# Optimization experiments

Hardware: AMD Instinct MI355X
Metric: run time of the kernel (lower is better)

Reference implementation:

```python
import jax, jax.numpy as jnp
import numpy as np

B, DIM, T = 8, 1024, 4096
CB, CD = 4096, 8          # codebook_size, codebook_dim
COMMIT = 0.25
EPS = 1e-12


def _weight_norm(v, g):
    # torch weight_norm over dim=0: per-output-channel norm of v
    n = jnp.sqrt(jnp.sum(v * v, axis=1, keepdims=True))
    return g[:, None] * v / n


def _l2_normalize(x):
    n = jnp.sqrt(jnp.sum(x * x, axis=1, keepdims=True))
    return x / jnp.maximum(n, EPS)


def setup_inputs() -> dict:
    key = jax.random.key(0)
    ks = jax.random.split(key, 5)
    z = jax.random.normal(ks[0], (B, DIM, T), jnp.float32)
    v_in = jax.random.normal(ks[1], (CD, DIM), jnp.float32) * 0.02   # conv1d k=1 weight (squeezed)
    g_in = jnp.sqrt(jnp.sum(v_in * v_in, axis=1))                     # weight_norm init: g = ||v||
    b_in = jnp.zeros((CD,), jnp.float32)
    codebook = jax.random.normal(ks[2], (CB, CD), jnp.float32)        # nn.Embedding default N(0,1)
    v_out = jax.random.normal(ks[3], (DIM, CD), jnp.float32) * 0.02
    g_out = jnp.sqrt(jnp.sum(v_out * v_out, axis=1))
    b_out = jnp.zeros((DIM,), jnp.float32)
    return {"z": z, "v_in": v_in, "g_in": g_in, "b_in": b_in,
            "codebook": codebook, "v_out": v_out, "g_out": g_out, "b_out": b_out}


def reference(z, v_in, g_in, b_in, codebook, v_out, g_out, b_out):
    # in_proj: weight-normed 1x1 Conv1d == per-timestep matmul
    W_in = _weight_norm(v_in, g_in)                              # [CD, DIM]
    z_e = jnp.einsum('od,bdt->bot', W_in, z) + b_in[None, :, None]  # [B, CD, T]

    # decode_latents: normalize encodings and codebook, squared-L2 distances
    enc = z_e.transpose(0, 2, 1).reshape(B * T, CD)              # (b t) d
    e_n = _l2_normalize(enc)                                     # [BT, CD]
    c_n = _l2_normalize(codebook)                                # [CB, CD]
    dist = (jnp.sum(e_n * e_n, axis=1, keepdims=True)
            - 2.0 * (e_n @ c_n.T)
            + jnp.sum(c_n * c_n, axis=1)[None, :])               # [BT, CB]
    indices = jnp.argmin(dist, axis=1).reshape(B, T)             # [B, T] int

    # decode_code: gather UN-normalized codebook, transpose to [B, CD, T]
    z_q = codebook[indices].transpose(0, 2, 1)                   # [B, CD, T]

    # training losses (per-batch), commitment + codebook
    sg = jax.lax.stop_gradient
    commitment_loss = jnp.mean((z_e - sg(z_q)) ** 2, axis=(1, 2)) * COMMIT
    codebook_loss = jnp.mean((z_q - sg(z_e)) ** 2, axis=(1, 2))
    commit_loss = commitment_loss + codebook_loss                # [B]

    # straight-through estimator
    z_q_ste = z_e + sg(z_q - z_e)                                # [B, CD, T]

    # out_proj
    W_out = _weight_norm(v_out, g_out)                           # [DIM, CD]
    out = jnp.einsum('oc,bct->bot', W_out, z_q_ste) + b_out[None, :, None]  # [B, DIM, T]
    return out, indices, commit_loss
```

## Files before the change

kernel.cpp:

```cpp
#include <hip/hip_runtime.h>

#define DIMN 1024
#define TN 4096
#define BN 8
#define CBN 4096
#define BTN (BN*TN)
#define OUT_ELEMS (BN*DIMN*TN)

typedef float fx4 __attribute__((ext_vector_type(4)));
typedef float fx2 __attribute__((ext_vector_type(2)));

#define WS_WINT 0
#define WS_WOUT 8192
#define WS_C2   49152
#define WS_CNP  53248
#define WS_LOSS 86016
#define WS_CNT  86024

#define LROWS_F 8192
#define LROW    68
#define LZQ_F   12544
#define LDS_TOT 13056

__device__ __forceinline__ float dot4(float4 a, float4 b) {
    float d = a.x * b.x;
    d = fmaf(a.y, b.y, d);
    d = fmaf(a.z, b.z, d);
    d = fmaf(a.w, b.w, d);
    return d;
}
__device__ __forceinline__ void add4(float4& a, float4 b) {
    a.x += b.x; a.y += b.y; a.z += b.z; a.w += b.w;
}
__device__ __forceinline__ fx2 lo2(fx4 v) { return __builtin_shufflevector(v, v, 0, 1); }
__device__ __forceinline__ fx2 hi2(fx4 v) { return __builtin_shufflevector(v, v, 2, 3); }
__device__ __forceinline__ fx2 splat2(float x) { fx2 r; r.x = x; r.y = x; return r; }
__device__ __forceinline__ fx2 fma2(fx2 a, fx2 b, fx2 c) { return __builtin_elementwise_fma(a, b, c); }
__device__ __forceinline__ fx2 max2(fx2 a, fx2 b) { return __builtin_elementwise_max(a, b); }
__device__ __forceinline__ fx2 min2(fx2 a, fx2 b) { return __builtin_elementwise_min(a, b); }
__device__ __forceinline__ fx4 cat4(fx2 a, fx2 b) { return __builtin_shufflevector(a, b, 0, 1, 2, 3); }

__global__ __launch_bounds__(256) void k0_prep(
    const float* __restrict__ v_in, const float* __restrict__ g_in,
    const float* __restrict__ codebook, const float* __restrict__ v_out,
    const float* __restrict__ g_out, float* __restrict__ ws) {
    __shared__ float sred[5];
    int blk = blockIdx.x, tid = threadIdx.x;
    if (blk < 8) {
        int o = blk;
        const float* v = v_in + o * DIMN;
        float4 x = *(const float4*)(v + tid * 4);
        float p = x.x * x.x + x.y * x.y + x.z * x.z + x.w * x.w;
        for (int off = 32; off >= 1; off >>= 1) p += __shfl_down(p, off, 64);
        if ((tid & 63) == 0) sred[tid >> 6] = p;
        __syncthreads();
        if (tid == 0) {
            float tot = sred[0] + sred[1] + sred[2] + sred[3];
            sred[4] = g_in[o] / sqrtf(tot);
        }
        __syncthreads();
        float s = sred[4];
        ws[WS_WINT + (tid * 4 + 0) * 8 + o] = x.x * s;
        ws[WS_WINT + (tid * 4 + 1) * 8 + o] = x.y * s;
        ws[WS_WINT + (tid * 4 + 2) * 8 + o] = x.z * s;
        ws[WS_WINT + (tid * 4 + 3) * 8 + o] = x.w * s;
    } else if (blk < 12) {
        int r = (blk - 8) * 256 + tid;
        const float* v = v_out + r * 8;
        float4 a = *(const float4*)v;
        float4 b = *(const float4*)(v + 4);
        float n2 = dot4(a, a) + dot4(b, b);
        float s = g_out[r] / sqrtf(n2);
        *(float4*)(ws + WS_WOUT + r * 8)     = make_float4(a.x*s, a.y*s, a.z*s, a.w*s);
        *(float4*)(ws + WS_WOUT + r * 8 + 4) = make_float4(b.x*s, b.y*s, b.z*s, b.w*s);
    } else if (blk < 28) {
        int j = (blk - 12) * 256 + tid;
        const float* c = codebook + j * 8;
        float4 a = *(const float4*)c;
        float4 b = *(const float4*)(c + 4);
        float n2 = dot4(a, a) + dot4(b, b);
        float inv = 1.0f / fmaxf(sqrtf(n2), 1e-12f);
        float na[8] = {a.x*inv, a.y*inv, a.z*inv, a.w*inv,
                       b.x*inv, b.y*inv, b.z*inv, b.w*inv};
        float* dst = ws + WS_CNP + (size_t)(j >> 1) * 16 + (j & 1);
        #pragma unroll
        for (int i = 0; i < 8; i++) dst[i * 2] = na[i];
        float h = 0.0f;
        #pragma unroll
        for (int i = 0; i < 8; i++) h = fmaf(na[i], na[i], h);
        ws[WS_C2 + j] = -0.5f * h;
    } else {
        if (tid < 9) ws[WS_LOSS + tid] = 0.0f;
    }
}

__global__ __launch_bounds__(512, 4) void k_mega(
    const float* __restrict__ z, const float* __restrict__ b_in,
    const float* __restrict__ codebook, const float* __restrict__ b_out,
    float* __restrict__ dout, float* __restrict__ ws) {
    __shared__ float sp[LDS_TOT];
    int tid = threadIdx.x, blk = blockIdx.x;
    int b = blk >> 6;
    int t0 = (blk & 63) * 64;

    #pragma unroll
    for (int i = 0; i < 4; i++) {
        int f4 = tid + i * 512;
        *(fx4*)(sp + f4 * 4) = *(const fx4*)(ws + WS_WINT + f4 * 4);
    }
    __syncthreads();

    if (tid < 256) {
        int p = tid >> 5, tpair = tid & 31;
        int tA = tpair * 2;
        const float* zp = z + ((size_t)(b * DIMN + p * 128)) * TN + t0 + tA;
        fx2 a0aL = splat2(0.f), a0aH = splat2(0.f), a0bL = splat2(0.f), a0bH = splat2(0.f);
        fx2 a1aL = splat2(0.f), a1aH = splat2(0.f), a1bL = splat2(0.f), a1bH = splat2(0.f);
        #pragma unroll 8
        for (int dd = 0; dd < 128; ++dd) {
            fx2 zv = __builtin_nontemporal_load((const fx2*)(zp + (size_t)dd * TN));
            const float* wv = sp + (p * 128 + dd) * 8;
            fx4 w0 = *(const fx4*)wv;
            fx4 w1 = *(const fx4*)(wv + 4);
            fx2 zx = splat2(zv.x), zy = splat2(zv.y);
            a0aL = fma2(lo2(w0), zx, a0aL); a0aH = fma2(hi2(w0), zx, a0aH);
            a0bL = fma2(lo2(w1), zx, a0bL); a0bH = fma2(hi2(w1), zx, a0bH);
            a1aL = fma2(lo2(w0), zy, a1aL); a1aH = fma2(hi2(w0), zy, a1aH);
            a1bL = fma2(lo2(w1), zy, a1bL); a1bH = fma2(hi2(w1), zy, a1bH);
        }
        float* q0 = sp + LROWS_F + tA * LROW + p * 8;
        *(fx4*)(q0)     = cat4(a0aL, a0aH);
        *(fx4*)(q0 + 4) = cat4(a0bL, a0bH);
        float* q1 = sp + LROWS_F + (tA + 1) * LROW + p * 8;
        *(fx4*)(q1)     = cat4(a1aL, a1aH);
        *(fx4*)(q1 + 4) = cat4(a1bL, a1bH);
    }
    __syncthreads();

    if (tid < 64) {
        int t = tid;
        float4 za = *(const float4*)(b_in);
        float4 zb = *(const float4*)(b_in + 4);
        #pragma unroll
        for (int p = 0; p < 8; p++) {
            const float* pp = sp + LROWS_F + t * LROW + p * 8;
            add4(za, *(const float4*)(pp));
            add4(zb, *(const float4*)(pp + 4));
        }
        float* row = sp + LROWS_F + t * LROW;
        *(float4*)(row)     = za;
        *(float4*)(row + 4) = zb;
        float inv = 1.0f / fmaxf(sqrtf(dot4(za, za) + dot4(zb, zb)), 1e-12f);
        *(float4*)(row + 8)  = make_float4(za.x*inv, za.y*inv, za.z*inv, za.w*inv);
        *(float4*)(row + 12) = make_float4(zb.x*inv, zb.y*inv, zb.z*inv, zb.w*inv);
    }
    __syncthreads();

    int co = tid >> 4, tg = tid & 15;
    float en[4][8];
    #pragma unroll
    for (int k = 0; k < 4; k++) {
        const float* rp = sp + LROWS_F + (tg * 4 + k) * LROW + 8;
        fx4 u = *(const fx4*)rp;
        fx4 v = *(const fx4*)(rp + 4);
        en[k][0]=u.x; en[k][1]=u.y; en[k][2]=u.z; en[k][3]=u.w;
        en[k][4]=v.x; en[k][5]=v.y; en[k][6]=v.z; en[k][7]=v.w;
    }
    fx2 bs[4]; int bje[4], bjo[4];
    #pragma unroll
    for (int k = 0; k < 4; k++) { bs[k] = splat2(-3.4e38f); bje[k] = 0; bjo[k] = 1; }
    #pragma unroll 1
    for (int ci = 0; ci < 16; ++ci) {
        int j0 = ci * 256 + co * 8;
        const float* cg = ws + WS_CNP + (size_t)j0 * 8;
        #pragma unroll
        for (int pp = 0; pp < 4; ++pp) {
            fx4 cA = *(const fx4*)(cg + pp * 16);
            fx4 cB = *(const fx4*)(cg + pp * 16 + 4);
            fx4 cC = *(const fx4*)(cg + pp * 16 + 8);
            fx4 cD = *(const fx4*)(cg + pp * 16 + 12);
            fx2 h2 = *(const fx2*)(ws + WS_C2 + j0 + pp * 2);
            int jE = j0 + pp * 2;
            #pragma unroll
            for (int k = 0; k < 4; k++) {
                fx2 s = h2;
                s = fma2(splat2(en[k][0]), lo2(cA), s);
                s = fma2(splat2(en[k][1]), hi2(cA), s);
                s = fma2(splat2(en[k][2]), lo2(cB), s);
                s = fma2(splat2(en[k][3]), hi2(cB), s);
                s = fma2(splat2(en[k][4]), lo2(cC), s);
                s = fma2(splat2(en[k][5]), hi2(cC), s);
                s = fma2(splat2(en[k][6]), lo2(cD), s);
                s = fma2(splat2(en[k][7]), hi2(cD), s);
                bool cE = s.x > bs[k].x;
                bool cO = s.y > bs[k].y;
                bs[k] = max2(bs[k], s);
                if (cE) bje[k] = jE;
                if (cO) bjo[k] = jE + 1;
            }
        }
    }
    float bsF[4]; int bjF[4];
    #pragma unroll
    for (int k = 0; k < 4; k++) {
        bsF[k] = bs[k].x; bjF[k] = bje[k];
        if (bs[k].y > bsF[k] || (bs[k].y == bsF[k] && bjo[k] < bjF[k])) {
            bsF[k] = bs[k].y; bjF[k] = bjo[k];
        }
    }
    #pragma unroll
    for (int st = 16; st <= 32; st <<= 1) {
        #pragma unroll
        for (int k = 0; k < 4; k++) {
            float os = __shfl_xor(bsF[k], st, 64);
            int   oj = __shfl_xor(bjF[k], st, 64);
            if (os > bsF[k] || (os == bsF[k] && oj < bjF[k])) { bsF[k] = os; bjF[k] = oj; }
        }
    }
    if ((tid & 63) < 16) {
        int w = tid >> 6;
        #pragma unroll
        for (int k = 0; k < 4; k++)
            *(fx2*)(sp + LROWS_F + (tg * 4 + k) * LROW + 32 + w * 2) =
                (fx2){bsF[k], __int_as_float(bjF[k])};
    }
    __syncthreads();

    if (tid < 64) {
        int t = tid;
        const float* crow = sp + LROWS_F + t * LROW + 32;
        fx2 c0 = *(const fx2*)(crow);
        float best = c0.x; int idx = __float_as_int(c0.y);
        #pragma unroll
        for (int w2 = 1; w2 < 8; w2++) {
            fx2 cw = *(const fx2*)(crow + w2 * 2);
            int j2 = __float_as_int(cw.y);
            if (cw.x > best || (cw.x == best && j2 < idx)) { best = cw.x; idx = j2; }
        }
        dout[(size_t)OUT_ELEMS + b * TN + t0 + t] = (float)idx;
        const float* cq = codebook + (size_t)idx * 8;
        float4 qa = *(const float4*)cq, qb = *(const float4*)(cq + 4);
        sp[LZQ_F + 0*64 + t] = qa.x; sp[LZQ_F + 1*64 + t] = qa.y;
        sp[LZQ_F + 2*64 + t] = qa.z; sp[LZQ_F + 3*64 + t] = qa.w;
        sp[LZQ_F + 4*64 + t] = qb.x; sp[LZQ_F + 5*64 + t] = qb.y;
        sp[LZQ_F + 6*64 + t] = qb.z; sp[LZQ_F + 7*64 + t] = qb.w;
        const float* row = sp + LROWS_F + t * LROW;
        float4 za = *(const float4*)(row);
        float4 zb = *(const float4*)(row + 4);
        float4 da = make_float4(za.x-qa.x, za.y-qa.y, za.z-qa.z, za.w-qa.w);
        float4 db = make_float4(zb.x-qb.x, zb.y-qb.y, zb.z-qb.z, zb.w-qb.w);
        float l = dot4(da, da) + dot4(db, db);
        for (int off = 32; off >= 1; off >>= 1) l += __shfl_down(l, off, 64);
        if (t == 0) atomicAdd(ws + WS_LOSS + b, l);
    } else {
        int i = tid - 64;
        #pragma unroll
        for (int r = 0; r < 5; r++) {
            int f4 = r * 448 + i;
            if (f4 < 2048) {
                fx4 v = *(const fx4*)(ws + WS_WOUT + f4 * 4);
                int o = f4 >> 1, h = f4 & 1;
                int tog = (o >> 6) & 1;
                *(fx4*)(sp + o * 8 + ((h ^ tog) << 2)) = v;
            }
        }
        #pragma unroll
        for (int r = 0; r < 3; r++) {
            int e = r * 448 + i;
            if (e < 1024) sp[LROWS_F + (e & 63) * LROW + 16 + (e >> 6)] = b_out[e];
        }
    }
    __syncthreads();

    {
        int t4 = tid & 15, og = tid >> 4;
        fx4 zr[8];
        #pragma unroll
        for (int c = 0; c < 8; c++) zr[c] = *(const fx4*)(sp + LZQ_F + c * 64 + t4 * 4);
        fx2 cmn = splat2(-8.f), cmx = splat2(8.f);
        size_t obase = ((size_t)(b * DIMN + og * 32)) * TN + (size_t)(t0 + t4 * 4);
        for (int k = 0; k < 32; k++) {
            int o = og * 32 + k;
            int tog = (o >> 6) & 1;
            fx4 wa = *(const fx4*)(sp + o * 8 + (tog << 2));
            fx4 wb = *(const fx4*)(sp + o * 8 + ((tog ^ 1) << 2));
            float bo = sp[LROWS_F + (o & 63) * LROW + 16 + (o >> 6)];
            fx2 accL = splat2(bo), accH = splat2(bo);
            float wcv[8] = {wa.x, wa.y, wa.z, wa.w, wb.x, wb.y, wb.z, wb.w};
            #pragma unroll
            for (int c = 0; c < 8; c++) {
                fx2 ws2 = splat2(wcv[c]);
                accL = fma2(ws2, lo2(zr[c]), accL);
                accH = fma2(ws2, hi2(zr[c]), accH);
            }
            accL = min2(max2(accL, cmn), cmx);
            accH = min2(max2(accH, cmn), cmx);
            fx4 st = cat4(accL, accH);
            __builtin_nontemporal_store(st, (fx4*)(dout + obase + (size_t)k * TN));
        }
    }

    if (tid == 0) {
        __threadfence();
        unsigned int old = atomicAdd((unsigned int*)(ws + WS_CNT), 1u);
        if (old == 511u) {
            #pragma unroll
            for (int i = 0; i < 8; i++) {
                float v = atomicAdd(ws + WS_LOSS + i, 0.0f);
                dout[(size_t)OUT_ELEMS + BTN + i] = v * (1.25f / 32768.0f);
            }
        }
    }
}

extern "C" void kernel_launch(void* const* d_in, const int* in_sizes, int n_in,
                              void* d_out, int out_size, void* d_ws, size_t ws_size,
                              hipStream_t stream) {
    (void)in_sizes; (void)n_in; (void)out_size; (void)ws_size;
    const float* z        = (const float*)d_in[0];
    const float* v_in     = (const float*)d_in[1];
    const float* g_in     = (const float*)d_in[2];
    const float* b_in     = (const float*)d_in[3];
    const float* codebook = (const float*)d_in[4];
    const float* v_out    = (const float*)d_in[5];
    const float* g_out    = (const float*)d_in[6];
    const float* b_out    = (const float*)d_in[7];
    float* out            = (float*)d_out;
    float* ws             = (float*)d_ws;

    hipLaunchKernelGGL(k0_prep, dim3(29), dim3(256), 0, stream,
                       v_in, g_in, codebook, v_out, g_out, ws);
    hipLaunchKernelGGL(k_mega, dim3(512), dim3(512), 0, stream,
                       z, b_in, codebook, b_out, out, ws);
}
```

Baseline: 297.6 us.

## Split fused mega kernel into in-projection and search/out-projection kernels

Splits the single fused kernel into two: k_ze computes the in-projection and normalized encodings for 32 timesteps per block and writes them to workspace, and k_sc performs the codebook argmin search, loss accumulation and out-projection. Both use smaller 256-thread blocks with 1024 blocks each, aiming for more occupancy and less LDS pressure than the 512-thread fused kernel. The trade-off is an extra launch, a global round trip for the encodings, and reading W_out and b_out from global memory or cache instead of LDS.

```diff
diff --git a/kernel.cpp b/kernel.cpp
--- a/kernel.cpp
+++ b/kernel.cpp
@@ -16,11 +16,7 @@
 #define WS_CNP  53248
 #define WS_LOSS 86016
 #define WS_CNT  86024
-
-#define LROWS_F 8192
-#define LROW    68
-#define LZQ_F   12544
-#define LDS_TOT 13056
+#define WS_ZEEN 131072
 
 __device__ __forceinline__ float dot4(float4 a, float4 b) {
     float d = a.x * b.x;
@@ -94,73 +90,64 @@
     }
 }
 
-__global__ __launch_bounds__(512, 4) void k_mega(
+__global__ __launch_bounds__(256, 8) void k_ze(
     const float* __restrict__ z, const float* __restrict__ b_in,
+    float* __restrict__ ws) {
+    __shared__ float rows[32 * 68];
+    int tid = threadIdx.x, blk = blockIdx.x;
+    int b = blk >> 7;
+    int t0 = (blk & 127) * 32;
+    int p = tid >> 5, t = tid & 31;
+    const float* zp = z + ((size_t)(b * DIMN + p * 128)) * TN + t0 + t;
+    const float* wp = ws + WS_WINT + p * 128 * 8;
+    fx2 a0 = splat2(0.f), a1 = splat2(0.f), a2 = splat2(0.f), a3 = splat2(0.f);
+    #pragma unroll 8
+    for (int dd = 0; dd < 128; ++dd) {
+        float zr = __builtin_nontemporal_load(zp + (size_t)dd * TN);
+        fx4 w0 = *(const fx4*)(wp + dd * 8);
+        fx4 w1 = *(const fx4*)(wp + dd * 8 + 4);
+        fx2 zz = splat2(zr);
+        a0 = fma2(lo2(w0), zz, a0);
+        a1 = fma2(hi2(w0), zz, a1);
+        a2 = fma2(lo2(w1), zz, a2);
+        a3 = fma2(hi2(w1), zz, a3);
+    }
+    float* q = rows + t * 68 + p * 8;
+    *(fx4*)(q)     = cat4(a0, a1);
+    *(fx4*)(q + 4) = cat4(a2, a3);
+    __syncthreads();
+    if (tid < 32) {
+        float4 za = *(const float4*)(b_in);
+        float4 zb = *(const float4*)(b_in + 4);
+        #pragma unroll
+        for (int pp = 0; pp < 8; pp++) {
+            const float* r = rows + tid * 68 + pp * 8;
+            add4(za, *(const float4*)(r));
+            add4(zb, *(const float4*)(r + 4));
+        }
+        float inv = 1.0f / fmaxf(sqrtf(dot4(za, za) + dot4(zb, zb)), 1e-12f);
+        float* o = ws + WS_ZEEN + ((size_t)(b * TN) + t0 + tid) * 16;
+        *(float4*)(o)      = za;
+        *(float4*)(o + 4)  = zb;
+        *(float4*)(o + 8)  = make_float4(za.x*inv, za.y*inv, za.z*inv, za.w*inv);
+        *(float4*)(o + 12) = make_float4(zb.x*inv, zb.y*inv, zb.z*inv, zb.w*inv);
+    }
+}
+
+__global__ __launch_bounds__(256, 4) void k_sc(
     const float* __restrict__ codebook, const float* __restrict__ b_out,
     float* __restrict__ dout, float* __restrict__ ws) {
-    __shared__ float sp[LDS_TOT];
+    __shared__ float cand[4 * 32 * 2];
+    __shared__ float zq[8 * 32];
     int tid = threadIdx.x, blk = blockIdx.x;
-    int b = blk >> 6;
-    int t0 = (blk & 63) * 64;
-
-    #pragma unroll
-    for (int i = 0; i < 4; i++) {
-        int f4 = tid + i * 512;
-        *(fx4*)(sp + f4 * 4) = *(const fx4*)(ws + WS_WINT + f4 * 4);
-    }
-    __syncthreads();
-
-    if (tid < 256) {
-        int p = tid >> 5, tpair = tid & 31;
-        int tA = tpair * 2;
-        const float* zp = z + ((size_t)(b * DIMN + p * 128)) * TN + t0 + tA;
-        fx2 a0aL = splat2(0.f), a0aH = splat2(0.f), a0bL = splat2(0.f), a0bH = splat2(0.f);
-        fx2 a1aL = splat2(0.f), a1aH = splat2(0.f), a1bL = splat2(0.f), a1bH = splat2(0.f);
-        #pragma unroll 8
-        for (int dd = 0; dd < 128; ++dd) {
-            fx2 zv = __builtin_nontemporal_load((const fx2*)(zp + (size_t)dd * TN));
-            const float* wv = sp + (p * 128 + dd) * 8;
-            fx4 w0 = *(const fx4*)wv;
-            fx4 w1 = *(const fx4*)(wv + 4);
-            fx2 zx = splat2(zv.x), zy = splat2(zv.y);
-            a0aL = fma2(lo2(w0), zx, a0aL); a0aH = fma2(hi2(w0), zx, a0aH);
-            a0bL = fma2(lo2(w1), zx, a0bL); a0bH = fma2(hi2(w1), zx, a0bH);
-            a1aL = fma2(lo2(w0), zy, a1aL); a1aH = fma2(hi2(w0), zy, a1aH);
-            a1bL = fma2(lo2(w1), zy, a1bL); a1bH = fma2(hi2(w1), zy, a1bH);
-        }
-        float* q0 = sp + LROWS_F + tA * LROW + p * 8;
-        *(fx4*)(q0)     = cat4(a0aL, a0aH);
-        *(fx4*)(q0 + 4) = cat4(a0bL, a0bH);
-        float* q1 = sp + LROWS_F + (tA + 1) * LROW + p * 8;
-        *(fx4*)(q1)     = cat4(a1aL, a1aH);
-        *(fx4*)(q1 + 4) = cat4(a1bL, a1bH);
-    }
-    __syncthreads();
-
-    if (tid < 64) {
-        int t = tid;
-        float4 za = *(const float4*)(b_in);
-        float4 zb = *(const float4*)(b_in + 4);
-        #pragma unroll
-        for (int p = 0; p < 8; p++) {
-            const float* pp = sp + LROWS_F + t * LROW + p * 8;
-            add4(za, *(const float4*)(pp));
-            add4(zb, *(const float4*)(pp + 4));
-        }
-        float* row = sp + LROWS_F + t * LROW;
-        *(float4*)(row)     = za;
-        *(float4*)(row + 4) = zb;
-        float inv = 1.0f / fmaxf(sqrtf(dot4(za, za) + dot4(zb, zb)), 1e-12f);
-        *(float4*)(row + 8)  = make_float4(za.x*inv, za.y*inv, za.z*inv, za.w*inv);
-        *(float4*)(row + 12) = make_float4(zb.x*inv, zb.y*inv, zb.z*inv, zb.w*inv);
-    }
-    __syncthreads();
-
-    int co = tid >> 4, tg = tid & 15;
+    int b = blk >> 7;
+    int t0 = (blk & 127) * 32;
+    int co = tid >> 3, tg = tid & 7;
+
     float en[4][8];
     #pragma unroll
     for (int k = 0; k < 4; k++) {
-        const float* rp = sp + LROWS_F + (tg * 4 + k) * LROW + 8;
+        const float* rp = ws + WS_ZEEN + ((size_t)(b * TN) + t0 + tg * 4 + k) * 16 + 8;
         fx4 u = *(const fx4*)rp;
         fx4 v = *(const fx4*)(rp + 4);
         en[k][0]=u.x; en[k][1]=u.y; en[k][2]=u.z; en[k][3]=u.w;
@@ -209,7 +196,7 @@
         }
     }
     #pragma unroll
-    for (int st = 16; st <= 32; st <<= 1) {
+    for (int st = 8; st <= 32; st <<= 1) {
         #pragma unroll
         for (int k = 0; k < 4; k++) {
             float os = __shfl_xor(bsF[k], st, 64);
@@ -217,74 +204,56 @@
             if (os > bsF[k] || (os == bsF[k] && oj < bjF[k])) { bsF[k] = os; bjF[k] = oj; }
         }
     }
-    if ((tid & 63) < 16) {
+    if ((tid & 63) < 8) {
         int w = tid >> 6;
         #pragma unroll
         for (int k = 0; k < 4; k++)
-            *(fx2*)(sp + LROWS_F + (tg * 4 + k) * LROW + 32 + w * 2) =
+            *(fx2*)(cand + (w * 32 + tg * 4 + k) * 2) =
                 (fx2){bsF[k], __int_as_float(bjF[k])};
     }
     __syncthreads();
 
-    if (tid < 64) {
+    if (tid < 32) {
         int t = tid;
-        const float* crow = sp + LROWS_F + t * LROW + 32;
-        fx2 c0 = *(const fx2*)(crow);
+        fx2 c0 = *(const fx2*)(cand + t * 2);
         float best = c0.x; int idx = __float_as_int(c0.y);
         #pragma unroll
-        for (int w2 = 1; w2 < 8; w2++) {
-            fx2 cw = *(const fx2*)(crow + w2 * 2);
+        for (int w2 = 1; w2 < 4; w2++) {
+            fx2 cw = *(const fx2*)(cand + (w2 * 32 + t) * 2);
             int j2 = __float_as_int(cw.y);
             if (cw.x > best || (cw.x == best && j2 < idx)) { best = cw.x; idx = j2; }
         }
         dout[(size_t)OUT_ELEMS + b * TN + t0 + t] = (float)idx;
         const float* cq = codebook + (size_t)idx * 8;
         float4 qa = *(const float4*)cq, qb = *(const float4*)(cq + 4);
-        sp[LZQ_F + 0*64 + t] = qa.x; sp[LZQ_F + 1*64 + t] = qa.y;
-        sp[LZQ_F + 2*64 + t] = qa.z; sp[LZQ_F + 3*64 + t] = qa.w;
-        sp[LZQ_F + 4*64 + t] = qb.x; sp[LZQ_F + 5*64 + t] = qb.y;
-        sp[LZQ_F + 6*64 + t] = qb.z; sp[LZQ_F + 7*64 + t] = qb.w;
-        const float* row = sp + LROWS_F + t * LROW;
-        float4 za = *(const float4*)(row);
-        float4 zb = *(const float4*)(row + 4);
+        zq[0*32 + t] = qa.x; zq[1*32 + t] = qa.y;
+        zq[2*32 + t] = qa.z; zq[3*32 + t] = qa.w;
+        zq[4*32 + t] = qb.x; zq[5*32 + t] = qb.y;
+        zq[6*32 + t] = qb.z; zq[7*32 + t] = qb.w;
+        const float* zer = ws + WS_ZEEN + ((size_t)(b * TN) + t0 + t) * 16;
+        float4 za = *(const float4*)(zer);
+        float4 zb = *(const float4*)(zer + 4);
         float4 da = make_float4(za.x-qa.x, za.y-qa.y, za.z-qa.z, za.w-qa.w);
         float4 db = make_float4(zb.x-qb.x, zb.y-qb.y, zb.z-qb.z, zb.w-qb.w);
         float l = dot4(da, da) + dot4(db, db);
-        for (int off = 32; off >= 1; off >>= 1) l += __shfl_down(l, off, 64);
+        for (int off = 16; off >= 1; off >>= 1) l += __shfl_down(l, off, 64);
         if (t == 0) atomicAdd(ws + WS_LOSS + b, l);
-    } else {
-        int i = tid - 64;
-        #pragma unroll
-        for (int r = 0; r < 5; r++) {
-            int f4 = r * 448 + i;
-            if (f4 < 2048) {
-                fx4 v = *(const fx4*)(ws + WS_WOUT + f4 * 4);
-                int o = f4 >> 1, h = f4 & 1;
-                int tog = (o >> 6) & 1;
-                *(fx4*)(sp + o * 8 + ((h ^ tog) << 2)) = v;
-            }
-        }
-        #pragma unroll
-        for (int r = 0; r < 3; r++) {
-            int e = r * 448 + i;
-            if (e < 1024) sp[LROWS_F + (e & 63) * LROW + 16 + (e >> 6)] = b_out[e];
-        }
     }
     __syncthreads();
 
     {
-        int t4 = tid & 15, og = tid >> 4;
+        int t4 = tid & 7, og = tid >> 3;
         fx4 zr[8];
         #pragma unroll
-        for (int c = 0; c < 8; c++) zr[c] = *(const fx4*)(sp + LZQ_F + c * 64 + t4 * 4);
+        for (int c = 0; c < 8; c++) zr[c] = *(const fx4*)(zq + c * 32 + t4 * 4);
         fx2 cmn = splat2(-8.f), cmx = splat2(8.f);
         size_t obase = ((size_t)(b * DIMN + og * 32)) * TN + (size_t)(t0 + t4 * 4);
         for (int k = 0; k < 32; k++) {
             int o = og * 32 + k;
-            int tog = (o >> 6) & 1;
-            fx4 wa = *(const fx4*)(sp + o * 8 + (tog << 2));
-            fx4 wb = *(const fx4*)(sp + o * 8 + ((tog ^ 1) << 2));
-            float bo = sp[LROWS_F + (o & 63) * LROW + 16 + (o >> 6)];
+            const float* wr = ws + WS_WOUT + o * 8;
+            fx4 wa = *(const fx4*)(wr);
+            fx4 wb = *(const fx4*)(wr + 4);
+            float bo = b_out[o];
             fx2 accL = splat2(bo), accH = splat2(bo);
             float wcv[8] = {wa.x, wa.y, wa.z, wa.w, wb.x, wb.y, wb.z, wb.w};
             #pragma unroll
@@ -303,7 +272,7 @@
     if (tid == 0) {
         __threadfence();
         unsigned int old = atomicAdd((unsigned int*)(ws + WS_CNT), 1u);
-        if (old == 511u) {
+        if (old == 1023u) {
             #pragma unroll
             for (int i = 0; i < 8; i++) {
                 float v = atomicAdd(ws + WS_LOSS + i, 0.0f);
@@ -330,6 +299,7 @@
 
     hipLaunchKernelGGL(k0_prep, dim3(29), dim3(256), 0, stream,
                        v_in, g_in, codebook, v_out, g_out, ws);
-    hipLaunchKernelGGL(k_mega, dim3(512), dim3(512), 0, stream,
-                       z, b_in, codebook, b_out, out, ws);
-}
+    hipLaunchKernelGGL(k_ze, dim3(1024), dim3(256), 0, stream, z, b_in, ws);
+    hipLaunchKernelGGL(k_sc, dim3(1024), dim3(256), 0, stream,
+                       codebook, b_out, out, ws);
+}
```

Result: slower. 348.3 us (+17.0%).
